# Performance work log

Measured on AMD Instinct MI355X. Metric: run time of the kernel, lower is better.

Reference implementation:

```python
import jax, jax.numpy as jnp
import numpy as np


def setup_inputs() -> dict:
    key = jax.random.key(0)
    k1, k2, k3, k4, k5 = jax.random.split(key, 5)
    B, D, H, W, C = 2, 16, 16, 16, 256
    x = jax.random.normal(k1, (B, D, H, W, C), dtype=jnp.float32)
    Wf = jax.random.normal(k2, (C, C // 4), dtype=jnp.float32) * (1.0 / np.sqrt(C))
    Wg = jax.random.normal(k3, (C, C // 4), dtype=jnp.float32) * (1.0 / np.sqrt(C))
    Wh = jax.random.normal(k4, (C, C), dtype=jnp.float32) * (1.0 / np.sqrt(C))
    gamma = jax.random.normal(k5, (1,), dtype=jnp.float32) * 0.1
    return {"x": x, "Wf": Wf, "Wg": Wg, "Wh": Wh, "gamma": gamma}


def reference(x, Wf, Wg, Wh, gamma):
    B, D, H, W, C = x.shape
    N = D * H * W
    xf = x.reshape(B, N, C)  # hw_flatten of input (1x1x1 conv == per-position matmul)
    f = jnp.einsum('bnc,cf->bnf', xf, Wf)   # [B, N, C//4]
    g = jnp.einsum('bnc,cf->bnf', xf, Wg)   # [B, N, C//4]
    h = jnp.einsum('bnc,cf->bnf', xf, Wh)   # [B, N, C]
    s = jnp.einsum('bnf,bmf->bnm', g, f)    # g @ f^T, [B, N, N]
    beta = jax.nn.softmax(s, axis=-1)
    o = jnp.einsum('bnm,bmc->bnc', beta, h)  # [B, N, C]
    out = gamma * o.reshape(B, D, H, W, C) + x
    beta_out = beta.reshape(-1, D, H, W, 1)  # [B*N, D, H, W, 1] as in original
    return (out, beta_out)
```

## Files before the change

### kernel.cpp

```cpp
#include <hip/hip_runtime.h>

#define NPOS 4096
#define CDIM 256
#define FDIM 64

typedef short short8 __attribute__((ext_vector_type(8)));
typedef float f32x4 __attribute__((ext_vector_type(4)));

__device__ __forceinline__ unsigned short f2bf(float v) {
  unsigned u = __float_as_uint(v);
  unsigned r = (u + 0x7fffu + ((u >> 16) & 1u)) >> 16;
  return (unsigned short)r;
}
__device__ __forceinline__ float bf2f(unsigned short u) {
  return __uint_as_float((unsigned)u << 16);
}
__device__ __forceinline__ short8 as_s8(uint4 u) {
  return *reinterpret_cast<short8*>(&u);
}
__device__ __forceinline__ void gload_lds16(const void* g, void* l) {
  __builtin_amdgcn_global_load_lds(
      (const __attribute__((address_space(1))) unsigned int*)g,
      (__attribute__((address_space(3))) unsigned int*)l, 16, 0, 0);
}

__global__ __launch_bounds__(256) void proj_kernel(
    const float* __restrict__ x, const float* __restrict__ Wf,
    const float* __restrict__ Wg, const float* __restrict__ Wh,
    unsigned short* __restrict__ f_hi, unsigned short* __restrict__ f_lo,
    unsigned short* __restrict__ g_hi, unsigned short* __restrict__ g_lo,
    unsigned short* __restrict__ h_t) {
  __shared__ float xs[16][CDIM];
  const int row0 = blockIdx.x * 16;
  const int t = threadIdx.x;
  {
    const float4* xv = reinterpret_cast<const float4*>(x + (size_t)row0 * CDIM);
    float4* sv = reinterpret_cast<float4*>(&xs[0][0]);
#pragma unroll
    for (int i = 0; i < 4; ++i) sv[t + 256 * i] = xv[t + 256 * i];
  }
  __syncthreads();
  {
    float acc[16];
#pragma unroll
    for (int r = 0; r < 16; ++r) acc[r] = 0.f;
    for (int k = 0; k < CDIM; k += 4) {
      const float w0 = Wh[(size_t)(k + 0) * CDIM + t];
      const float w1 = Wh[(size_t)(k + 1) * CDIM + t];
      const float w2 = Wh[(size_t)(k + 2) * CDIM + t];
      const float w3 = Wh[(size_t)(k + 3) * CDIM + t];
#pragma unroll
      for (int r = 0; r < 16; ++r) {
        const float4 xv = *reinterpret_cast<const float4*>(&xs[r][k]);
        float a = acc[r];
        a = fmaf(xv.x, w0, a);
        a = fmaf(xv.y, w1, a);
        a = fmaf(xv.z, w2, a);
        a = fmaf(xv.w, w3, a);
        acc[r] = a;
      }
    }
    const int b = row0 >> 12;
    const int lr = row0 & (NPOS - 1);
    unsigned wd[8];
#pragma unroll
    for (int i = 0; i < 8; ++i)
      wd[i] = (unsigned)f2bf(acc[2 * i]) | ((unsigned)f2bf(acc[2 * i + 1]) << 16);
    uint4* base = reinterpret_cast<uint4*>(h_t + ((size_t)(b * CDIM + t)) * NPOS);
    const int m = t & 7;
    const int c0 = lr >> 3;
    base[c0 ^ m] = make_uint4(wd[0], wd[1], wd[2], wd[3]);
    base[(c0 + 1) ^ m] = make_uint4(wd[4], wd[5], wd[6], wd[7]);
  }
  {
    const int col = t & 63;
    const int rb = (t >> 6) * 4;
    const int colq = col >> 3, cwi = col & 7;
    float af[4] = {0.f, 0.f, 0.f, 0.f};
    float ag[4] = {0.f, 0.f, 0.f, 0.f};
    for (int k = 0; k < CDIM; k += 4) {
      const float wf0 = Wf[(size_t)(k + 0) * FDIM + col];
      const float wf1 = Wf[(size_t)(k + 1) * FDIM + col];
      const float wf2 = Wf[(size_t)(k + 2) * FDIM + col];
      const float wf3 = Wf[(size_t)(k + 3) * FDIM + col];
      const float wg0 = Wg[(size_t)(k + 0) * FDIM + col];
      const float wg1 = Wg[(size_t)(k + 1) * FDIM + col];
      const float wg2 = Wg[(size_t)(k + 2) * FDIM + col];
      const float wg3 = Wg[(size_t)(k + 3) * FDIM + col];
#pragma unroll
      for (int r = 0; r < 4; ++r) {
        const float4 xv = *reinterpret_cast<const float4*>(&xs[rb + r][k]);
        float a = af[r], bb = ag[r];
        a = fmaf(xv.x, wf0, a); a = fmaf(xv.y, wf1, a);
        a = fmaf(xv.z, wf2, a); a = fmaf(xv.w, wf3, a);
        bb = fmaf(xv.x, wg0, bb); bb = fmaf(xv.y, wg1, bb);
        bb = fmaf(xv.z, wg2, bb); bb = fmaf(xv.w, wg3, bb);
        af[r] = a; ag[r] = bb;
      }
    }
#pragma unroll
    for (int r = 0; r < 4; ++r) {
      const int row = row0 + rb + r;
      const int ph = ((colq ^ (row & 7)) << 3) | cwi;
      const size_t of = (size_t)row * FDIM + ph;
      const size_t og = (size_t)row * FDIM + col;
      const unsigned short fh = f2bf(af[r]);
      const unsigned short gh = f2bf(ag[r]);
      f_hi[of] = fh;
      f_lo[of] = f2bf(af[r] - bf2f(fh));
      g_hi[og] = gh;
      g_lo[og] = f2bf(ag[r] - bf2f(gh));
    }
  }
}

__global__ __launch_bounds__(512, 4) void attn_fused_kernel(
    const unsigned short* __restrict__ f_hi, const unsigned short* __restrict__ f_lo,
    const unsigned short* __restrict__ g_hi, const unsigned short* __restrict__ g_lo,
    const unsigned short* __restrict__ h_t, const float* __restrict__ x,
    const float* __restrict__ gamma, float* __restrict__ beta,
    float* __restrict__ out) {
  __shared__ __align__(16) char shraw[69632];
  __shared__ float partl[8][16];
  __shared__ float linvs[16];
  uint4 (*Fh)[128][8] = reinterpret_cast<uint4(*)[128][8]>(shraw);
  uint4 (*Fl)[128][8] = reinterpret_cast<uint4(*)[128][8]>(shraw + 32768);
  uint4 (*Ab)[16][8] = reinterpret_cast<uint4(*)[16][8]>(shraw);
  uint4 (*Bb)[256][8] = reinterpret_cast<uint4(*)[256][8]>(shraw + 4096);

  const int wg = blockIdx.x;
  const int wgid = (wg & 7) * 64 + (wg >> 3);
  const int b = wgid >> 8;
  const int row0 = (wgid & 255) * 16;
  const int t = threadIdx.x;
  const int w = t >> 6;
  const int l = t & 63;
  const int lr = l & 15;
  const int lk = l >> 4;

  const int arow = row0 + lr;
  short8 gh[2], gl[2];
  {
    const unsigned short* gH = g_hi + ((size_t)(b * NPOS + arow)) * FDIM + lk * 8;
    const unsigned short* gL = g_lo + ((size_t)(b * NPOS + arow)) * FDIM + lk * 8;
#pragma unroll
    for (int ks = 0; ks < 2; ++ks) {
      gh[ks] = *reinterpret_cast<const short8*>(gH + ks * 32);
      gl[ks] = *reinterpret_cast<const short8*>(gL + ks * 32);
    }
  }
  const unsigned short* fbh = f_hi + (size_t)b * NPOS * FDIM;
  const unsigned short* fbl = f_lo + (size_t)b * NPOS * FDIM;
  unsigned short* Pb = (unsigned short*)(beta + (size_t)b * NPOS * NPOS);
  unsigned short* prow = Pb + (size_t)arow * (2 * NPOS) + NPOS;
  const int rsw = lr & 7;
  float lsum = 0.f;

#define STAGEA(buf, tile)                                                      \
  do {                                                                         \
    const int tile0_ = (tile) * 128;                                           \
    _Pragma("unroll")                                                          \
    for (int j = 0; j < 2; ++j) {                                              \
      const int slot_ = j * 512 + t;                                           \
      const int row_ = slot_ >> 3, ch_ = slot_ & 7;                            \
      gload_lds16(fbh + (size_t)(tile0_ + row_) * FDIM + ch_ * 8,              \
                  (char*)&Fh[buf][0][0] + (size_t)slot_ * 16);                 \
      gload_lds16(fbl + (size_t)(tile0_ + row_) * FDIM + ch_ * 8,              \
                  (char*)&Fl[buf][0][0] + (size_t)slot_ * 16);                 \
    }                                                                          \
  } while (0)

  STAGEA(0, 0);
  asm volatile("s_waitcnt vmcnt(0) lgkmcnt(0)\ns_barrier" ::: "memory");

  const int rrA = w * 16 + lr;
  const int fsw = rrA & 7;
  int buf = 0;
  for (int tile = 0; tile < 32; ++tile) {
    if (tile < 31) STAGEA(buf ^ 1, tile + 1);
    __builtin_amdgcn_sched_barrier(0);
    const uint4 h0 = Fh[buf][rrA][lk ^ fsw];
    const uint4 h1 = Fh[buf][rrA][(lk + 4) ^ fsw];
    const uint4 q0 = Fl[buf][rrA][lk ^ fsw];
    const uint4 q1 = Fl[buf][rrA][(lk + 4) ^ fsw];
    f32x4 acca = {0.f, 0.f, 0.f, 0.f};
    f32x4 accb = {0.f, 0.f, 0.f, 0.f};
    acca = __builtin_amdgcn_mfma_f32_16x16x32_bf16(as_s8(h0), gh[0], acca, 0, 0, 0);
    accb = __builtin_amdgcn_mfma_f32_16x16x32_bf16(as_s8(h0), gl[0], accb, 0, 0, 0);
    acca = __builtin_amdgcn_mfma_f32_16x16x32_bf16(as_s8(q0), gh[0], acca, 0, 0, 0);
    accb = __builtin_amdgcn_mfma_f32_16x16x32_bf16(as_s8(h1), gh[1], accb, 0, 0, 0);
    acca = __builtin_amdgcn_mfma_f32_16x16x32_bf16(as_s8(q1), gh[1], acca, 0, 0, 0);
    accb = __builtin_amdgcn_mfma_f32_16x16x32_bf16(as_s8(h1), gl[1], accb, 0, 0, 0);
    const f32x4 acc = acca + accb;
    const int cq = tile * 128 + w * 16 + lk * 4;
    const float e0 = __expf(acc[0]);
    const float e1 = __expf(acc[1]);
    const float e2 = __expf(acc[2]);
    const float e3 = __expf(acc[3]);
    lsum += (e0 + e1) + (e2 + e3);
    uint2 pk;
    pk.x = (unsigned)f2bf(e0) | ((unsigned)f2bf(e1) << 16);
    pk.y = (unsigned)f2bf(e2) | ((unsigned)f2bf(e3) << 16);
    const int sidx = (((cq >> 3) ^ rsw) << 3) | (cq & 7);
    *reinterpret_cast<uint2*>(prow + sidx) = pk;
    asm volatile("s_waitcnt vmcnt(1) lgkmcnt(0)\ns_barrier" ::: "memory");
    buf ^= 1;
  }
#undef STAGEA

  lsum += __shfl_xor(lsum, 16);
  lsum += __shfl_xor(lsum, 32);
  if (l < 16) partl[w][l] = lsum;
  __syncthreads();
  if (t < 16) {
    float s = 0.f;
#pragma unroll
    for (int q = 0; q < 8; ++q) s += partl[q][t];
    linvs[t] = __frcp_rn(s);
  }
  asm volatile("s_waitcnt vmcnt(0) lgkmcnt(0)\ns_barrier" ::: "memory");

  const size_t hoff = (size_t)b * CDIM * NPOS;
  const unsigned short* Pub = (const unsigned short*)(beta + (size_t)b * NPOS * NPOS);

#define STAGEB(buf, kt)                                                         \
  do {                                                                          \
    _Pragma("unroll")                                                           \
    for (int j = 0; j < 4; ++j) {                                               \
      const int slot_ = j * 512 + t;                                            \
      const unsigned short* g_ = h_t + hoff + (size_t)(slot_ >> 3) * NPOS +     \
                                 (size_t)((kt) * 8 + (slot_ & 7)) * 8;          \
      gload_lds16(g_, (char*)&Bb[buf][0][0] + (size_t)slot_ * 16);              \
    }                                                                           \
    if (t < 128) {                                                              \
      const unsigned short* g_ = Pub + (size_t)(row0 + (t >> 3)) * (2 * NPOS) + \
                                 NPOS + (size_t)((kt) * 8 + (t & 7)) * 8;       \
      gload_lds16(g_, (char*)&Ab[buf][0][0] + (size_t)t * 16);                  \
    }                                                                           \
  } while (0)

  f32x4 acc0 = {0.f, 0.f, 0.f, 0.f}, acc1 = {0.f, 0.f, 0.f, 0.f};
  const int c0 = w * 32 + lr;
  const int c1 = c0 + 16;
  const int brow = t >> 5;
  const int jj = t & 31;

  STAGEB(0, 0);
  asm volatile("s_waitcnt vmcnt(0) lgkmcnt(0)\ns_barrier" ::: "memory");

  buf = 0;
  for (int kt = 0; kt < 64; ++kt) {
    if (kt < 63) STAGEB(buf ^ 1, kt + 1);
    __builtin_amdgcn_sched_barrier(0);
    {
      const uint4 a0 = Ab[buf][lr][lk ^ (lr & 7)];
      const uint4 a1 = Ab[buf][lr][(4 + lk) ^ (lr & 7)];
      const uint4 b00 = Bb[buf][c0][lk ^ (c0 & 7)];
      const uint4 b01 = Bb[buf][c1][lk ^ (c1 & 7)];
      const uint4 b10 = Bb[buf][c0][(4 + lk) ^ (c0 & 7)];
      const uint4 b11 = Bb[buf][c1][(4 + lk) ^ (c1 & 7)];
      acc0 = __builtin_amdgcn_mfma_f32_16x16x32_bf16(as_s8(a0), as_s8(b00), acc0, 0, 0, 0);
      acc1 = __builtin_amdgcn_mfma_f32_16x16x32_bf16(as_s8(a0), as_s8(b01), acc1, 0, 0, 0);
      acc0 = __builtin_amdgcn_mfma_f32_16x16x32_bf16(as_s8(a1), as_s8(b10), acc0, 0, 0, 0);
      acc1 = __builtin_amdgcn_mfma_f32_16x16x32_bf16(as_s8(a1), as_s8(b11), acc1, 0, 0, 0);
    }
    {
      const float il = linvs[brow];
      const unsigned* arow_ = reinterpret_cast<const unsigned*>(&Ab[buf][brow][0]);
      const unsigned u = arow_[(((jj >> 2) ^ (brow & 7)) << 2) | (jj & 3)];
      float2 v;
      v.x = bf2f((unsigned short)(u & 0xffffu)) * il;
      v.y = bf2f((unsigned short)(u >> 16)) * il;
      *reinterpret_cast<float2*>(beta + (size_t)(b * NPOS + row0 + brow) * NPOS +
                                 (size_t)kt * 64 + jj * 2) = v;
    }
    asm volatile("s_waitcnt vmcnt(1) lgkmcnt(0)\ns_barrier" ::: "memory");
    buf ^= 1;
  }
#undef STAGEB

  const float gam = gamma[0];
#pragma unroll
  for (int r = 0; r < 4; ++r) {
    const int lrr = lk * 4 + r;
    const int orow = row0 + lrr;
    const float sc = gam * linvs[lrr];
    const size_t i0 = ((size_t)b * NPOS + orow) * CDIM + w * 32 + lr;
    out[i0] = fmaf(sc, acc0[r], x[i0]);
    out[i0 + 16] = fmaf(sc, acc1[r], x[i0 + 16]);
  }
}

extern "C" void kernel_launch(void* const* d_in, const int* in_sizes, int n_in,
                              void* d_out, int out_size, void* d_ws, size_t ws_size,
                              hipStream_t stream) {
  (void)in_sizes; (void)n_in; (void)out_size; (void)ws_size;
  const float* x = (const float*)d_in[0];
  const float* Wf = (const float*)d_in[1];
  const float* Wg = (const float*)d_in[2];
  const float* Wh = (const float*)d_in[3];
  const float* gamma = (const float*)d_in[4];

  float* out = (float*)d_out;
  float* beta = out + (size_t)2 * NPOS * CDIM;

  unsigned short* h_t = (unsigned short*)d_ws;
  unsigned short* f_hi = h_t + (size_t)2 * CDIM * NPOS;
  unsigned short* f_lo = f_hi + (size_t)2 * NPOS * FDIM;
  unsigned short* g_hi = f_lo + (size_t)2 * NPOS * FDIM;
  unsigned short* g_lo = g_hi + (size_t)2 * NPOS * FDIM;

  hipLaunchKernelGGL(proj_kernel, dim3(2 * NPOS / 16), dim3(256), 0, stream,
                     x, Wf, Wg, Wh, f_hi, f_lo, g_hi, g_lo, h_t);
  hipLaunchKernelGGL(attn_fused_kernel, dim3(512), dim3(512), 0, stream,
                     f_hi, f_lo, g_hi, g_lo, h_t, x, gamma, beta, out);
}
```

Measured before the change: 133.4 us.

## Deepen phase-B prefetch to four stages with half-width k-tiles and new swizzle

Replaces the double-buffered P·H loop (64-wide k tiles, 64 iterations) with a 4-buffer ring of 32-wide k tiles prefetched three tiles ahead over 128 iterations. The LDS layouts for the beta-stash (A) and h_t (B) tiles are re-swizzled so each lane reads one contiguous chunk. The per-row inverse sum is hoisted out of the loop. The intent is to hide global-to-LDS latency behind more in-flight loads. In exchange it doubles the barriers and issues wasted loads at the tail. The vmcnt thresholds assume a fixed per-thread load count, which may not hold for threads that issue only the B loads.

```diff
diff --git a/kernel.cpp b/kernel.cpp
--- a/kernel.cpp
+++ b/kernel.cpp
@@ -125,8 +125,8 @@
   __shared__ float linvs[16];
   uint4 (*Fh)[128][8] = reinterpret_cast<uint4(*)[128][8]>(shraw);
   uint4 (*Fl)[128][8] = reinterpret_cast<uint4(*)[128][8]>(shraw + 32768);
-  uint4 (*Ab)[16][8] = reinterpret_cast<uint4(*)[16][8]>(shraw);
-  uint4 (*Bb)[256][8] = reinterpret_cast<uint4(*)[256][8]>(shraw + 4096);
+  uint4 (*Ab)[64] = reinterpret_cast<uint4(*)[64]>(shraw);
+  uint4 (*Bb)[1024] = reinterpret_cast<uint4(*)[1024]>(shraw + 4096);
 
   const int wg = blockIdx.x;
   const int wgid = (wg & 7) * 64 + (wg >> 3);
@@ -223,19 +223,23 @@
   const size_t hoff = (size_t)b * CDIM * NPOS;
   const unsigned short* Pub = (const unsigned short*)(beta + (size_t)b * NPOS * NPOS);
 
-#define STAGEB(buf, kt)                                                         \
+#define STAGEB(bufi, kt)                                                        \
   do {                                                                          \
     _Pragma("unroll")                                                           \
-    for (int j = 0; j < 4; ++j) {                                               \
+    for (int j = 0; j < 2; ++j) {                                               \
       const int slot_ = j * 512 + t;                                            \
-      const unsigned short* g_ = h_t + hoff + (size_t)(slot_ >> 3) * NPOS +     \
-                                 (size_t)((kt) * 8 + (slot_ & 7)) * 8;          \
-      gload_lds16(g_, (char*)&Bb[buf][0][0] + (size_t)slot_ * 16);              \
+      const int col_ = slot_ & 255, ch_ = slot_ >> 8;                           \
+      const unsigned short* g_ = h_t + hoff + (size_t)col_ * NPOS +             \
+                                 (size_t)(((kt) * 4 + ch_) ^ (col_ & 7)) * 8;   \
+      gload_lds16(g_, (char*)&Bb[bufi][0] + (size_t)slot_ * 16);                \
     }                                                                           \
-    if (t < 128) {                                                              \
-      const unsigned short* g_ = Pub + (size_t)(row0 + (t >> 3)) * (2 * NPOS) + \
-                                 NPOS + (size_t)((kt) * 8 + (t & 7)) * 8;       \
-      gload_lds16(g_, (char*)&Ab[buf][0][0] + (size_t)t * 16);                  \
+    if (t < 64) {                                                               \
+      const int row_ = t >> 2, chL_ = t & 3;                                    \
+      const int o_ = chL_ ^ ((row_ >> 1) & 3);                                  \
+      const int g4_ = ((kt) * 4 + o_) ^ (row_ & 7);                             \
+      const unsigned short* g_ = Pub + (size_t)(row0 + row_) * (2 * NPOS) +     \
+                                 NPOS + (size_t)g4_ * 8;                        \
+      gload_lds16(g_, (char*)&Ab[bufi][0] + (size_t)t * 16);                    \
     }                                                                           \
   } while (0)
 
@@ -244,39 +248,41 @@
   const int c1 = c0 + 16;
   const int brow = t >> 5;
   const int jj = t & 31;
+  const float il_brow = linvs[brow];
+
+#define PHB_BODY(kt, WAITSTR)                                                   \
+  do {                                                                          \
+    STAGEB(((kt) + 3) & 3, ((kt) + 3) & 127);                                   \
+    __builtin_amdgcn_sched_barrier(0);           \
+    const int bufc_ = (kt) & 3;                                                 \
+    const uint4 a0_ = Ab[bufc_][lr * 4 + (lk ^ ((lr >> 1) & 3))];               \
+    const uint4 b00_ = Bb[bufc_][lk * 256 + c0];                                \
+    const uint4 b01_ = Bb[bufc_][lk * 256 + c1];                                \
+    acc0 = __builtin_amdgcn_mfma_f32_16x16x32_bf16(as_s8(a0_), as_s8(b00_),     \
+                                                   acc0, 0, 0, 0);              \
+    acc1 = __builtin_amdgcn_mfma_f32_16x16x32_bf16(as_s8(a0_), as_s8(b01_),     \
+                                                   acc1, 0, 0, 0);              \
+    {                                                                           \
+      const unsigned short* abr_ = (const unsigned short*)&Ab[bufc_][0];        \
+      const unsigned short u16_ =                                               \
+          abr_[(brow * 4 + ((jj >> 3) ^ ((brow >> 1) & 3))) * 8 + (jj & 7)];    \
+      beta[(size_t)(b * NPOS + row0 + brow) * NPOS + (kt) * 32 + jj] =          \
+          bf2f(u16_) * il_brow;                                                 \
+    }                                                                           \
+    asm volatile("s_waitcnt " WAITSTR " lgkmcnt(0)\ns_barrier" ::: "memory");   \
+  } while (0)
 
   STAGEB(0, 0);
-  asm volatile("s_waitcnt vmcnt(0) lgkmcnt(0)\ns_barrier" ::: "memory");
-
-  buf = 0;
-  for (int kt = 0; kt < 64; ++kt) {
-    if (kt < 63) STAGEB(buf ^ 1, kt + 1);
-    __builtin_amdgcn_sched_barrier(0);
-    {
-      const uint4 a0 = Ab[buf][lr][lk ^ (lr & 7)];
-      const uint4 a1 = Ab[buf][lr][(4 + lk) ^ (lr & 7)];
-      const uint4 b00 = Bb[buf][c0][lk ^ (c0 & 7)];
-      const uint4 b01 = Bb[buf][c1][lk ^ (c1 & 7)];
-      const uint4 b10 = Bb[buf][c0][(4 + lk) ^ (c0 & 7)];
-      const uint4 b11 = Bb[buf][c1][(4 + lk) ^ (c1 & 7)];
-      acc0 = __builtin_amdgcn_mfma_f32_16x16x32_bf16(as_s8(a0), as_s8(b00), acc0, 0, 0, 0);
-      acc1 = __builtin_amdgcn_mfma_f32_16x16x32_bf16(as_s8(a0), as_s8(b01), acc1, 0, 0, 0);
-      acc0 = __builtin_amdgcn_mfma_f32_16x16x32_bf16(as_s8(a1), as_s8(b10), acc0, 0, 0, 0);
-      acc1 = __builtin_amdgcn_mfma_f32_16x16x32_bf16(as_s8(a1), as_s8(b11), acc1, 0, 0, 0);
-    }
-    {
-      const float il = linvs[brow];
-      const unsigned* arow_ = reinterpret_cast<const unsigned*>(&Ab[buf][brow][0]);
-      const unsigned u = arow_[(((jj >> 2) ^ (brow & 7)) << 2) | (jj & 3)];
-      float2 v;
-      v.x = bf2f((unsigned short)(u & 0xffffu)) * il;
-      v.y = bf2f((unsigned short)(u >> 16)) * il;
-      *reinterpret_cast<float2*>(beta + (size_t)(b * NPOS + row0 + brow) * NPOS +
-                                 (size_t)kt * 64 + jj * 2) = v;
-    }
-    asm volatile("s_waitcnt vmcnt(1) lgkmcnt(0)\ns_barrier" ::: "memory");
-    buf ^= 1;
-  }
+  STAGEB(1, 1);
+  STAGEB(2, 2);
+  asm volatile("s_waitcnt vmcnt(4) lgkmcnt(0)\ns_barrier" ::: "memory");
+
+  PHB_BODY(0, "vmcnt(5)");
+  PHB_BODY(1, "vmcnt(6)");
+  for (int kt = 2; kt < 128; ++kt) {
+    PHB_BODY(kt, "vmcnt(7)");
+  }
+#undef PHB_BODY
 #undef STAGEB
 
   const float gam = gamma[0];
```

New measurement: 221.3 us. 66.0% more time.
